# Optimization experiments

Measured on AMD Instinct MI355X. Metric: run time of the kernel, lower is better.

Reference implementation:

```python
import jax, jax.numpy as jnp
import numpy as np

N = 100000      # nodes
E = 1600000     # edges (avg degree 16)
D_IN = 64
H1, H2, OUT = 64, 32, 2


def setup_inputs() -> dict:
    key = jax.random.key(0)
    ks = jax.random.split(key, 12)
    x = jax.random.normal(ks[0], (N, D_IN), jnp.float32)
    edge_index = jax.random.randint(ks[1], (2, E), 0, N, dtype=jnp.int32)

    def lin(k, fin, fout):
        return jax.random.normal(k, (fin, fout), jnp.float32) / np.sqrt(fin)

    return {
        "x": x,
        "edge_index": edge_index,
        # SAGEConv1: lin_l (neighbors, with bias) + lin_r (root, no bias)
        "Wl1": lin(ks[2], D_IN, H1), "bl1": jnp.zeros((H1,), jnp.float32),
        "Wr1": lin(ks[3], D_IN, H1),
        # SAGEConv2
        "Wl2": lin(ks[4], H1, H2), "bl2": jnp.zeros((H2,), jnp.float32),
        "Wr2": lin(ks[5], H1, H2),
        # final Linear(32, 2)
        "Wf": lin(ks[6], H2, OUT),
        "bf": jnp.zeros((OUT,), jnp.float32),
    }


def reference(x, edge_index, Wl1, bl1, Wr1, Wl2, bl2, Wr2, Wf, bf):
    src, dst = edge_index[0], edge_index[1]
    n = x.shape[0]
    # in-degree for mean aggregation (isolated nodes -> divide by 1, aggr stays 0)
    deg = jax.ops.segment_sum(jnp.ones(src.shape, x.dtype), dst, num_segments=n)
    inv_deg = 1.0 / jnp.maximum(deg, 1.0)

    def sage(h, Wl, bl, Wr):
        # gather source features, scatter-sum to targets, then mean
        aggr = jax.ops.segment_sum(h[src], dst, num_segments=n) * inv_deg[:, None]
        return aggr @ Wl + bl + h @ Wr  # lin_l(mean_neigh) + lin_r(root)

    h = jax.nn.relu(sage(x, Wl1, bl1, Wr1))
    h = jax.nn.relu(sage(h, Wl2, bl2, Wr2))
    return h @ Wf + bf
```

## Files before the change

### kernel.cpp

```cpp
#include <hip/hip_runtime.h>

#define NN 100000
#define EE 1600000
#define NB 391
#define BCAP 4608
#define BINB 640
#define EPB (EE / BINB)
#define NL1B ((NN + 63) / 64)
#define XCAST 1563
#define FGRID (BINB + XCAST + 16 + 4 + 2 + 1)

typedef unsigned int u32;
typedef unsigned short u16;
typedef __attribute__((ext_vector_type(8))) short bf16x8;
typedef __attribute__((ext_vector_type(4))) float f32x4;

__device__ __forceinline__ u32 f2bf(float f) {
    u32 u = __float_as_uint(f);
    return (u + 0x7fffu + ((u >> 16) & 1u)) >> 16;
}
__device__ __forceinline__ float bf_lo(u32 u) { return __uint_as_float(u << 16); }
__device__ __forceinline__ float bf_hi(u32 u) { return __uint_as_float(u & 0xffff0000u); }
__device__ __forceinline__ u32 pk2(float lo, float hi) { return f2bf(lo) | (f2bf(hi) << 16); }

__global__ __launch_bounds__(512) void kbinprep(const int* __restrict__ src,
                                                const int* __restrict__ dst,
                                                int* __restrict__ gcur,
                                                int* __restrict__ gbin,
                                                const float* __restrict__ x,
                                                const float* __restrict__ Wl1,
                                                const float* __restrict__ Wr1,
                                                const float* __restrict__ Wl2,
                                                const float* __restrict__ Wr2,
                                                u16* __restrict__ xb,
                                                u16* __restrict__ wbT,
                                                u16* __restrict__ w2T,
                                                u32* __restrict__ wr2p,
                                                u16* __restrict__ z2b) {
    __shared__ int lsp[EPB];
    __shared__ u16 lsb[EPB];
    __shared__ int ls2[EPB];
    __shared__ int lh[NB + 1];
    __shared__ int lcur[NB];
    __shared__ int lbase[NB];
    int tid = threadIdx.x;
    int b = blockIdx.x;
    if (b < BINB) {
        int e0 = b * EPB;
        for (int t = tid; t < NB; t += 512) { lh[t + 1] = 0; lcur[t] = 0; }
        if (tid == 0) lh[0] = 0;
        __syncthreads();
        for (int i = tid; i < EPB; i += 512) {
            int d = dst[e0 + i], s = src[e0 + i];
            lsp[i] = (s << 8) | (d & 255);
            int bb = d >> 8;
            lsb[i] = (u16)bb;
            atomicAdd(&lh[bb + 1], 1);
        }
        __syncthreads();
        for (int o = 1; o < NB; o <<= 1) {
            int v = 0;
            if (tid < NB && tid >= o) v = lh[tid - o + 1];
            __syncthreads();
            if (tid < NB) lh[tid + 1] += v;
            __syncthreads();
        }
        if (tid < NB) {
            int cnt = lh[tid + 1] - lh[tid];
            lbase[tid] = cnt ? atomicAdd(&gcur[tid], cnt) : 0;
        }
        __syncthreads();
        for (int i = tid; i < EPB; i += 512) {
            int bb = lsb[i];
            int pos = atomicAdd(&lcur[bb], 1);
            ls2[lh[bb] + pos] = lsp[i];
        }
        __syncthreads();
        for (int i = tid; i < EPB; i += 512) {
            int lo = 0, hi = NB - 1;
#pragma unroll
            for (int it = 0; it < 9; ++it) {
                int mid = (lo + hi + 1) >> 1;
                if (lh[mid] <= i) lo = mid; else hi = mid - 1;
            }
            int ib = lbase[lo] + (i - lh[lo]);
            if (ib < BCAP) gbin[(size_t)lo * BCAP + ib] = ls2[i];
        }
        return;
    }
    int b2 = b - BINB;
    if (b2 < XCAST) {
        int i = b2 * 512 + tid;
        if (i < NN * 64 / 8) {
            const float4* x4 = (const float4*)x;
            float4 a = x4[2 * i], c = x4[2 * i + 1];
            ((uint4*)xb)[i] = make_uint4(pk2(a.x, a.y), pk2(a.z, a.w),
                                         pk2(c.x, c.y), pk2(c.z, c.w));
        }
        return;
    }
    b2 -= XCAST;
    if (b2 < 16) {
        int idx = b2 * 512 + tid;
        int n = idx >> 7, k = idx & 127;
        float v = (k < 64) ? Wl1[k * 64 + n] : Wr1[(k - 64) * 64 + n];
        wbT[idx] = (u16)f2bf(v);
    } else if (b2 < 20) {
        int idx = (b2 - 16) * 512 + tid;
        int n = idx >> 6, k = idx & 63;
        w2T[idx] = (u16)f2bf(Wl2[k * 32 + n]);
    } else if (b2 < 22) {
        int idx = (b2 - 20) * 512 + tid;
        int k2 = idx >> 5, f = idx & 31;
        wr2p[idx] = pk2(Wr2[(2 * k2) * 32 + f], Wr2[(2 * k2 + 1) * 32 + f]);
    } else {
        if (tid < 32) ((u32*)(xb + (size_t)NN * 64))[tid] = 0;
        else if (tid < 48) ((u32*)(z2b + (size_t)NN * 32))[tid - 32] = 0;
    }
}

__global__ __launch_bounds__(512) void ksort(const int* __restrict__ gcur,
                                             const int* __restrict__ gbin,
                                             int* __restrict__ elist,
                                             int* __restrict__ offs,
                                             int* __restrict__ deg) {
    __shared__ int ls[BCAP];
    __shared__ int ls2[BCAP];
    __shared__ int lh0[256], lh[256], lcur[256];
    int tid = threadIdx.x;
    int b = blockIdx.x;
    int cnt = gcur[b]; if (cnt > BCAP) cnt = BCAP;
    const int* bin = gbin + (size_t)b * BCAP;
    for (int i = tid; i < cnt; i += 512) ls[i] = bin[i];
    if (tid < 256) { lh0[tid] = 0; lcur[tid] = 0; }
    __syncthreads();
    for (int i = tid; i < cnt; i += 512) atomicAdd(&lh0[ls[i] & 255], 1);
    __syncthreads();
    if (tid < 256) lh[tid] = lh0[tid];
    __syncthreads();
    for (int o = 1; o < 256; o <<= 1) {
        int v = 0;
        if (tid < 256 && tid >= o) v = lh[tid - o];
        __syncthreads();
        if (tid < 256) lh[tid] += v;
        __syncthreads();
    }
    for (int i = tid; i < cnt; i += 512) {
        int e = ls[i], d = e & 255;
        int pos = atomicAdd(&lcur[d], 1);
        ls2[lh[d] - lh0[d] + pos] = e >> 8;
    }
    __syncthreads();
    int boff = b * BCAP;
    for (int i = tid; i < cnt; i += 512) elist[boff + i] = ls2[i];
    int nodes = NN - b * 256; if (nodes > 256) nodes = 256;
    if (tid < nodes) {
        offs[b * 256 + tid] = boff + lh[tid] - lh0[tid];
        deg[b * 256 + tid] = lh0[tid];
    }
}

__global__ __launch_bounds__(256) void kaggr1(const u16* __restrict__ xb,
                                              const int* __restrict__ offs,
                                              const int* __restrict__ deg,
                                              const int* __restrict__ elist,
                                              u32* __restrict__ aggr1u) {
    int tid = threadIdx.x;
    int l32 = tid & 31;
    int g = tid >> 5;
    int node = blockIdx.x * 8 + g;
    int o0 = offs[node];
    int c = deg[node];
    float inv = 1.0f / fmaxf((float)c, 1.0f);
    if (c > 64) c = 64;
    int e0 = elist[o0 + l32];
    int e1 = elist[o0 + 32 + l32];
    const u32* xbu = (const u32*)xb;
    float aL = 0.f, aH = 0.f;
#define B16A(EREG, JB, CNT)                                                   \
    {                                                                         \
        _Pragma("unroll")                                                     \
        for (int j = 0; j < (CNT); ++j) {                                     \
            int jj = (JB) + j;                                                \
            int id = (jj < c) ? __shfl((EREG), jj & 31, 32) : NN;             \
            u32 u = xbu[(u32)id * 32 + l32];                                  \
            aL += bf_lo(u); aH += bf_hi(u);                                   \
        }                                                                     \
    }
    B16A(e0, 0, 16)
    if (c > 16) B16A(e0, 16, 8)
    if (c > 24) B16A(e0, 24, 8)
    if (c > 32) B16A(e1, 32, 8)
    if (c > 40) B16A(e1, 40, 8)
    if (c > 48) B16A(e1, 48, 8)
    if (c > 56) B16A(e1, 56, 8)
#undef B16A
    aggr1u[(size_t)node * 32 + l32] = pk2(aL * inv, aH * inv);
}

__global__ __launch_bounds__(256) void l1gemm(const u32* __restrict__ aggr1u,
                                              const u16* __restrict__ xb,
                                              const u16* __restrict__ wbT,
                                              const u16* __restrict__ w2T,
                                              const float* __restrict__ bl1,
                                              u16* __restrict__ rh,
                                              u16* __restrict__ z2b) {
    __shared__ u16 sWb[64][136];
    __shared__ u16 sW2[32][72];
    __shared__ u16 sA[64][136];
    __shared__ u16 sH[64][72];
    __shared__ float sbl[64];
    int tid = threadIdx.x;
    int node0 = blockIdx.x * 64;

    for (int idx = tid; idx < 4096; idx += 256) {
        int n = idx >> 6, j = idx & 63;
        ((u32*)&sWb[n][0])[j] = ((const u32*)wbT)[idx];
    }
    for (int idx = tid; idx < 1024; idx += 256) {
        int n = idx >> 5, j = idx & 31;
        ((u32*)&sW2[n][0])[j] = ((const u32*)w2T)[idx];
    }
    if (tid < 64) sbl[tid] = bl1[tid];
    const u32* xbu = (const u32*)xb;
    for (int idx = tid; idx < 2048; idx += 256) {
        int row = idx >> 5, j = idx & 31;
        int nd = node0 + row; if (nd > NN - 1) nd = NN - 1;
        u32* dstA = (u32*)&sA[row][0];
        dstA[j]      = aggr1u[(size_t)nd * 32 + j];
        dstA[32 + j] = xbu[(size_t)nd * 32 + j];
    }
    __syncthreads();

    int l = tid & 63, w = tid >> 6;
    int m = l & 15, sel = l >> 4;

    bf16x8 af[4];
#pragma unroll
    for (int kc = 0; kc < 4; ++kc)
        af[kc] = *(const bf16x8*)&sA[w * 16 + m][kc * 32 + sel * 8];

    f32x4 acc0 = {0.f, 0.f, 0.f, 0.f};
    f32x4 acc1 = acc0, acc2 = acc0, acc3 = acc0;
#pragma unroll
    for (int kc = 0; kc < 4; ++kc) {
        bf16x8 b0 = *(const bf16x8*)&sWb[0 + m][kc * 32 + sel * 8];
        bf16x8 b1 = *(const bf16x8*)&sWb[16 + m][kc * 32 + sel * 8];
        bf16x8 b2 = *(const bf16x8*)&sWb[32 + m][kc * 32 + sel * 8];
        bf16x8 b3 = *(const bf16x8*)&sWb[48 + m][kc * 32 + sel * 8];
        acc0 = __builtin_amdgcn_mfma_f32_16x16x32_bf16(af[kc], b0, acc0, 0, 0, 0);
        acc1 = __builtin_amdgcn_mfma_f32_16x16x32_bf16(af[kc], b1, acc1, 0, 0, 0);
        acc2 = __builtin_amdgcn_mfma_f32_16x16x32_bf16(af[kc], b2, acc2, 0, 0, 0);
        acc3 = __builtin_amdgcn_mfma_f32_16x16x32_bf16(af[kc], b3, acc3, 0, 0, 0);
    }
#pragma unroll
    for (int nt = 0; nt < 4; ++nt) {
        f32x4 a = (nt == 0) ? acc0 : (nt == 1) ? acc1 : (nt == 2) ? acc2 : acc3;
        int col = nt * 16 + m;
        float b = sbl[col];
#pragma unroll
        for (int r = 0; r < 4; ++r) {
            float h = fmaxf(a[r] + b, 0.f);
            sH[w * 16 + sel * 4 + r][col] = (u16)f2bf(h);
        }
    }
    __syncthreads();

    bf16x8 hf0 = *(const bf16x8*)&sH[w * 16 + m][0 + sel * 8];
    bf16x8 hf1 = *(const bf16x8*)&sH[w * 16 + m][32 + sel * 8];
    f32x4 z0 = {0.f, 0.f, 0.f, 0.f};
    f32x4 z1 = z0;
    {
        bf16x8 b00 = *(const bf16x8*)&sW2[0 + m][0 + sel * 8];
        bf16x8 b01 = *(const bf16x8*)&sW2[0 + m][32 + sel * 8];
        bf16x8 b10 = *(const bf16x8*)&sW2[16 + m][0 + sel * 8];
        bf16x8 b11 = *(const bf16x8*)&sW2[16 + m][32 + sel * 8];
        z0 = __builtin_amdgcn_mfma_f32_16x16x32_bf16(hf0, b00, z0, 0, 0, 0);
        z0 = __builtin_amdgcn_mfma_f32_16x16x32_bf16(hf1, b01, z0, 0, 0, 0);
        z1 = __builtin_amdgcn_mfma_f32_16x16x32_bf16(hf0, b10, z1, 0, 0, 0);
        z1 = __builtin_amdgcn_mfma_f32_16x16x32_bf16(hf1, b11, z1, 0, 0, 0);
    }
#pragma unroll
    for (int r = 0; r < 4; ++r) {
        int node = node0 + w * 16 + sel * 4 + r;
        if (node < NN) {
            z2b[(size_t)node * 32 + m]      = (u16)f2bf(z0[r]);
            z2b[(size_t)node * 32 + 16 + m] = (u16)f2bf(z1[r]);
        }
    }
    for (int idx = tid; idx < 2048; idx += 256) {
        int row = idx >> 5, j = idx & 31;
        int node = node0 + row;
        if (node < NN) ((u32*)rh)[(size_t)node * 32 + j] = *(const u32*)&sH[row][2 * j];
    }
}

__global__ __launch_bounds__(256) void l2fused(const u16* __restrict__ z2b,
                                               const int* __restrict__ offs,
                                               const int* __restrict__ deg,
                                               const int* __restrict__ elist,
                                               const u16* __restrict__ rh,
                                               const u32* __restrict__ wr2p,
                                               const float* __restrict__ bl2,
                                               const float* __restrict__ Wf,
                                               const float* __restrict__ bfin,
                                               float* __restrict__ out) {
    __shared__ u32 sWp[32][32];
    __shared__ float sWf[32][2];
    __shared__ float sh1[16][64];
    __shared__ float sa2[16][32];
    __shared__ float sh2[16][32];
    int tid = threadIdx.x;
    for (int t = tid; t < 1024; t += 256) ((u32*)sWp)[t] = wr2p[t];
    if (tid < 64) sWf[tid >> 1][tid & 1] = Wf[tid];
    const u32* rh32 = (const u32*)rh;
    for (int t = tid; t < 512; t += 256) {
        int g = t >> 5, j = t & 31;
        u32 u = rh32[((size_t)blockIdx.x * 16 + g) * 32 + j];
        sh1[g][2 * j] = bf_lo(u);
        sh1[g][2 * j + 1] = bf_hi(u);
    }

    {
        int l16 = tid & 15;
        int g = tid >> 4;
        int node = blockIdx.x * 16 + g;
        int o0 = offs[node];
        int c = deg[node];
        float inv = 1.0f / fmaxf((float)c, 1.0f);
        if (c > 64) c = 64;
        int e0 = elist[o0 + l16], e1 = elist[o0 + 16 + l16];
        int e2 = elist[o0 + 32 + l16], e3 = elist[o0 + 48 + l16];
        const u32* zu = (const u32*)z2b;
        float aL = 0.f, aH = 0.f;
#define B16B(EREG, JB, CNT)                                                   \
        {                                                                     \
            _Pragma("unroll")                                                 \
            for (int j = 0; j < (CNT); ++j) {                                 \
                int jj = (JB) + j;                                            \
                int id = (jj < c) ? __shfl((EREG), jj & 15, 16) : NN;         \
                u32 u = zu[(u32)id * 16 + l16];                               \
                aL += bf_lo(u); aH += bf_hi(u);                               \
            }                                                                 \
        }
        B16B(e0, 0, 16)
        if (c > 16) B16B(e1, 16, 8)
        if (c > 24) B16B(e1, 24, 8)
        if (c > 32) B16B(e2, 32, 8)
        if (c > 40) B16B(e2, 40, 8)
        if (c > 48) B16B(e3, 48, 8)
        if (c > 56) B16B(e3, 56, 8)
#undef B16B
        sa2[g][2 * l16]     = aL * inv;
        sa2[g][2 * l16 + 1] = aH * inv;
    }
    __syncthreads();

    int f2 = tid & 31, gg = tid >> 5;
    float b2 = bl2[f2];
    float p0 = sa2[gg][f2] + b2;
    float p1 = sa2[gg + 8][f2] + b2;
#pragma unroll
    for (int k2 = 0; k2 < 32; ++k2) {
        u32 w = sWp[k2][f2];
        float w0 = bf_lo(w), w1 = bf_hi(w);
        float2 aA = *(const float2*)&sh1[gg][2 * k2];
        float2 aB = *(const float2*)&sh1[gg + 8][2 * k2];
        p0 = fmaf(aA.x, w0, p0); p0 = fmaf(aA.y, w1, p0);
        p1 = fmaf(aB.x, w0, p1); p1 = fmaf(aB.y, w1, p1);
    }
    sh2[gg][f2] = fmaxf(p0, 0.f);
    sh2[gg + 8][f2] = fmaxf(p1, 0.f);
    __syncthreads();

    if (tid < 32) {
        int ng = tid >> 1, cc = tid & 1;
        float o = bfin[cc];
#pragma unroll
        for (int k = 0; k < 32; ++k) o = fmaf(sh2[ng][k], sWf[k][cc], o);
        out[((size_t)blockIdx.x * 16 + ng) * 2 + cc] = o;
    }
}

extern "C" void kernel_launch(void* const* d_in, const int* in_sizes, int n_in,
                              void* d_out, int out_size, void* d_ws, size_t ws_size,
                              hipStream_t stream) {
    const float* x   = (const float*)d_in[0];
    const int*   ei  = (const int*)d_in[1];
    const float* Wl1 = (const float*)d_in[2];
    const float* bl1 = (const float*)d_in[3];
    const float* Wr1 = (const float*)d_in[4];
    const float* Wl2 = (const float*)d_in[5];
    const float* bl2 = (const float*)d_in[6];
    const float* Wr2 = (const float*)d_in[7];
    const float* Wf  = (const float*)d_in[8];
    const float* bf  = (const float*)d_in[9];
    float* out = (float*)d_out;

    const int* src = ei;
    const int* dst = ei + EE;

    int*   gcur   = (int*)d_ws;
    int*   deg    = gcur + 512;
    int*   offs   = deg + NN;
    int*   gbin   = offs + NN;
    int*   elist  = gbin + (size_t)NB * BCAP + 64;
    u16*   xb     = (u16*)(elist + (size_t)NB * BCAP + 64);
    u16*   rh     = xb + (size_t)(NN + 1) * 64;
    u16*   z2b    = rh + (size_t)NN * 64;
    u32*   aggr1u = (u32*)(z2b + (size_t)(NN + 1) * 32);
    u16*   wbT    = (u16*)(aggr1u + (size_t)NN * 32);
    u16*   w2T    = wbT + 8192;
    u32*   wr2p   = (u32*)(w2T + 2048);

    hipMemsetAsync(gcur, 0, 512 * sizeof(int), stream);

    kbinprep<<<FGRID, 512, 0, stream>>>(src, dst, gcur, gbin,
                                        x, Wl1, Wr1, Wl2, Wr2,
                                        xb, wbT, w2T, wr2p, z2b);

    ksort<<<NB, 512, 0, stream>>>(gcur, gbin, elist, offs, deg);

    kaggr1<<<NN / 8, 256, 0, stream>>>(xb, offs, deg, elist, aggr1u);

    l1gemm<<<NL1B, 256, 0, stream>>>(aggr1u, xb, wbT, w2T, bl1, rh, z2b);

    l2fused<<<NN / 16, 256, 0, stream>>>(z2b, offs, deg, elist, rh, wr2p, bl2, Wf, bf, out);
}
```

Baseline: 121.0 us.

## Replace global atomic bin reservation with per-block count matrix and gather in sort

The binning kernel no longer reserves space in global per-bin counters with atomics. It writes its locally sorted chunk contiguously, plus a per-bin count and start offset into a count matrix. The sort kernel reads that matrix column, prefix-sums the 640 segment counts with a wave scan, and gathers each segment from all binning blocks. This removes the memset, the global atomics and the binary-search scatter, at the cost of reading the count matrix and doing many small strided gathers in ksort.

```diff
diff --git a/kernel.cpp b/kernel.cpp
--- a/kernel.cpp
+++ b/kernel.cpp
@@ -6,6 +6,7 @@
 #define BCAP 4608
 #define BINB 640
 #define EPB (EE / BINB)
+#define CSTRIDE 392
 #define NL1B ((NN + 63) / 64)
 #define XCAST 1563
 #define FGRID (BINB + XCAST + 16 + 4 + 2 + 1)
@@ -25,8 +26,9 @@
 
 __global__ __launch_bounds__(512) void kbinprep(const int* __restrict__ src,
                                                 const int* __restrict__ dst,
-                                                int* __restrict__ gcur,
                                                 int* __restrict__ gbin,
+                                                u16* __restrict__ cntm,
+                                                u16* __restrict__ sstm,
                                                 const float* __restrict__ x,
                                                 const float* __restrict__ Wl1,
                                                 const float* __restrict__ Wr1,
@@ -42,7 +44,6 @@
     __shared__ int ls2[EPB];
     __shared__ int lh[NB + 1];
     __shared__ int lcur[NB];
-    __shared__ int lbase[NB];
     int tid = threadIdx.x;
     int b = blockIdx.x;
     if (b < BINB) {
@@ -66,8 +67,8 @@
             __syncthreads();
         }
         if (tid < NB) {
-            int cnt = lh[tid + 1] - lh[tid];
-            lbase[tid] = cnt ? atomicAdd(&gcur[tid], cnt) : 0;
+            cntm[b * CSTRIDE + tid] = (u16)(lh[tid + 1] - lh[tid]);
+            sstm[b * CSTRIDE + tid] = (u16)lh[tid];
         }
         __syncthreads();
         for (int i = tid; i < EPB; i += 512) {
@@ -76,16 +77,8 @@
             ls2[lh[bb] + pos] = lsp[i];
         }
         __syncthreads();
-        for (int i = tid; i < EPB; i += 512) {
-            int lo = 0, hi = NB - 1;
-#pragma unroll
-            for (int it = 0; it < 9; ++it) {
-                int mid = (lo + hi + 1) >> 1;
-                if (lh[mid] <= i) lo = mid; else hi = mid - 1;
-            }
-            int ib = lbase[lo] + (i - lh[lo]);
-            if (ib < BCAP) gbin[(size_t)lo * BCAP + ib] = ls2[i];
-        }
+        for (int i = tid; i < EPB; i += 512)
+            gbin[e0 + i] = ls2[i];
         return;
     }
     int b2 = b - BINB;
@@ -119,7 +112,8 @@
     }
 }
 
-__global__ __launch_bounds__(512) void ksort(const int* __restrict__ gcur,
+__global__ __launch_bounds__(512) void ksort(const u16* __restrict__ cntm,
+                                             const u16* __restrict__ sstm,
                                              const int* __restrict__ gbin,
                                              int* __restrict__ elist,
                                              int* __restrict__ offs,
@@ -127,12 +121,45 @@
     __shared__ int ls[BCAP];
     __shared__ int ls2[BCAP];
     __shared__ int lh0[256], lh[256], lcur[256];
+    __shared__ int segoff[BINB + 1];
+    __shared__ u16 segc[BINB], segst[BINB];
     int tid = threadIdx.x;
     int b = blockIdx.x;
-    int cnt = gcur[b]; if (cnt > BCAP) cnt = BCAP;
-    const int* bin = gbin + (size_t)b * BCAP;
-    for (int i = tid; i < cnt; i += 512) ls[i] = bin[i];
+    for (int w = tid; w < BINB; w += 512) {
+        segc[w]  = cntm[w * CSTRIDE + b];
+        segst[w] = sstm[w * CSTRIDE + b];
+    }
     if (tid < 256) { lh0[tid] = 0; lcur[tid] = 0; }
+    __syncthreads();
+    if (tid < 64) {
+        int base = tid * 10;
+        int local[10];
+        int s = 0;
+#pragma unroll
+        for (int j = 0; j < 10; ++j) { local[j] = s; s += (int)segc[base + j]; }
+        int incl = s;
+        for (int o = 1; o < 64; o <<= 1) {
+            int v = __shfl_up(incl, o, 64);
+            if (tid >= o) incl += v;
+        }
+        int excl = incl - s;
+#pragma unroll
+        for (int j = 0; j < 10; ++j) segoff[base + j] = excl + local[j];
+        if (tid == 63) segoff[BINB] = incl;
+    }
+    __syncthreads();
+    int cnt = segoff[BINB]; if (cnt > BCAP) cnt = BCAP;
+    {
+        int grp = tid >> 3, lane = tid & 7;
+        for (int w = grp; w < BINB; w += 64) {
+            int c = segc[w], so = segoff[w];
+            int gs = w * EPB + segst[w];
+            for (int j = lane; j < c; j += 8) {
+                int di = so + j;
+                if (di < BCAP) ls[di] = gbin[gs + j];
+            }
+        }
+    }
     __syncthreads();
     for (int i = tid; i < cnt; i += 512) atomicAdd(&lh0[ls[i] & 255], 1);
     __syncthreads();
@@ -400,11 +427,10 @@
     const int* src = ei;
     const int* dst = ei + EE;
 
-    int*   gcur   = (int*)d_ws;
-    int*   deg    = gcur + 512;
+    int*   deg    = (int*)d_ws;
     int*   offs   = deg + NN;
     int*   gbin   = offs + NN;
-    int*   elist  = gbin + (size_t)NB * BCAP + 64;
+    int*   elist  = gbin + (size_t)BINB * EPB;
     u16*   xb     = (u16*)(elist + (size_t)NB * BCAP + 64);
     u16*   rh     = xb + (size_t)(NN + 1) * 64;
     u16*   z2b    = rh + (size_t)NN * 64;
@@ -412,14 +438,14 @@
     u16*   wbT    = (u16*)(aggr1u + (size_t)NN * 32);
     u16*   w2T    = wbT + 8192;
     u32*   wr2p   = (u32*)(w2T + 2048);
-
-    hipMemsetAsync(gcur, 0, 512 * sizeof(int), stream);
-
-    kbinprep<<<FGRID, 512, 0, stream>>>(src, dst, gcur, gbin,
+    u16*   cntm   = (u16*)(wr2p + 1024);
+    u16*   sstm   = cntm + (size_t)BINB * CSTRIDE;
+
+    kbinprep<<<FGRID, 512, 0, stream>>>(src, dst, gbin, cntm, sstm,
                                         x, Wl1, Wr1, Wl2, Wr2,
                                         xb, wbT, w2T, wr2p, z2b);
 
-    ksort<<<NB, 512, 0, stream>>>(gcur, gbin, elist, offs, deg);
+    ksort<<<NB, 512, 0, stream>>>(cntm, sstm, gbin, elist, offs, deg);
 
     kaggr1<<<NN / 8, 256, 0, stream>>>(xb, offs, deg, elist, aggr1u);
 
```

Result: faster. 110.4 us (-8.8%).
